# Kernel tuning notes

Measured on AMD Instinct MI355X. Metric: run time of the kernel, lower is better.

## Reference

```python
import jax, jax.numpy as jnp
import numpy as np
from jax import lax

# module hyperparameters (init_kwargs)
L2_U = 0.01
L2_V = 0.01
L1_RATIO = 0.1
EPS = 1e-16


def soft_thresholding(x, thr):
    return jnp.sign(x) * jnp.maximum(jnp.abs(x) - thr, 0.0)


def update_u(x, u, v, l1, l2):
    # x: [B, M, N], u: [B, M, R], v: [B, N, R]
    a = x @ v                              # [B, M, R]
    b = jnp.swapaxes(v, -1, -2) @ v        # [B, R, R]
    R = u.shape[-1]

    # Sequential coordinate descent over rank r; u_new carries the data
    # dependency. term2 over indices j != r equals u_new @ b[:, :, r]
    # minus the diagonal contribution u_new[:, :, r] * b[r, r].
    def step(u_new, r):
        a_r = lax.dynamic_slice_in_dim(a, r, 1, 2)        # [B, M, 1]
        b_col = lax.dynamic_slice_in_dim(b, r, 1, 2)      # [B, R, 1]
        b_rr = lax.dynamic_slice_in_dim(b_col, r, 1, 1)   # [B, 1, 1]
        u_r = lax.dynamic_slice_in_dim(u_new, r, 1, 2)    # [B, M, 1]
        term2 = u_new @ b_col - u_r * b_rr                # [B, M, 1]
        num = soft_thresholding(a_r - term2, l1)
        ur_new = num / (b_rr + l2 + EPS)                  # project = Identity
        u_new = lax.dynamic_update_slice_in_dim(u_new, ur_new, r, 2)
        return u_new, None

    u_new, _ = lax.scan(step, u, jnp.arange(R))
    return u_new


def setup_inputs() -> dict:
    key = jax.random.key(0)
    kx, ku, kv = jax.random.split(key, 3)
    B, M, N, R = 16, 2048, 2048, 64
    x = jax.random.normal(kx, (B, M, N), dtype=jnp.float32)
    u = jax.random.normal(ku, (B, M, R), dtype=jnp.float32)
    v = jax.random.normal(kv, (B, N, R), dtype=jnp.float32)
    return {"x": x, "u": u, "v": v}


def reference(x, u, v):
    M, N = x.shape[-2], x.shape[-1]
    l1_u = L2_U * L1_RATIO * N
    l2_u = L2_U * (1.0 - L1_RATIO) * N
    l1_v = L2_V * L1_RATIO * M
    l2_v = L2_V * (1.0 - L1_RATIO) * M
    u = update_u(x, u, v, l1_u, l2_u)                       # factor 0
    v = update_u(jnp.swapaxes(x, -1, -2), v, u, l1_v, l2_v)  # factor 1 (uses new u)
    return (u, v)
```

## Files before the change

kernel.cpp:

```cpp
#include <hip/hip_runtime.h>

typedef __attribute__((ext_vector_type(8))) short short8;
typedef __attribute__((ext_vector_type(4))) float f32x4;

#define BB 16
#define MM 2048
#define NN 2048

static __device__ __forceinline__ unsigned int cvtpk(float lo, float hi) {
  unsigned int r;
  asm("v_cvt_pk_bf16_f32 %0, %1, %2" : "=v"(r) : "v"(lo), "v"(hi));
  return r;
}

#define WAITV(N)                                            \
  do {                                                      \
    asm volatile("s_waitcnt vmcnt(" #N ")" ::: "memory");   \
    __builtin_amdgcn_sched_barrier(0);                      \
  } while (0)
#define BAR() __builtin_amdgcn_s_barrier()

__global__ void transpose_cvt(const float* __restrict__ in,
                              unsigned short* __restrict__ out, int nrows) {
  __shared__ float t[64][65];
  int b = blockIdx.y;
  int n0 = blockIdx.x * 64;
  int tid = threadIdx.x;
  int lane = tid & 63;
  int q = tid >> 6;
  const float* inb = in + ((size_t)b * nrows + n0) * 64;
#pragma unroll
  for (int i = 0; i < 16; ++i) {
    int n = q * 16 + i;
    t[n][lane] = inb[n * 64 + lane];
  }
  __syncthreads();
  unsigned short* outb = out + (size_t)b * 64 * nrows + n0;
  int pr = tid & 31, rq = tid >> 5;
#pragma unroll
  for (int i = 0; i < 8; ++i) {
    int r = rq + 8 * i;
    int n = 2 * pr;
    *(unsigned int*)(outb + (size_t)r * nrows + n) = cvtpk(t[n][r], t[n + 1][r]);
  }
}

#define CD_TAIL(U_OUT, L1, L2E)                                                 \
  __syncthreads();                                                              \
  float* lsa = (float*)smem;                              \
  float* lsb = (float*)(smem + 16384);                    \
  float* invv = (float*)(smem + 32768);                   \
  _Pragma("unroll")                                                             \
  for (int i = 0; i < 4; ++i) {                                                 \
    int ctv = (w + i) & 3;                                                      \
    _Pragma("unroll")                                                           \
    for (int j = 0; j < 4; ++j) {                                               \
      lsa[(w * 16 + 4 * g + j) * 64 + ctv * 16 + lr] = acc[i][j];               \
      lsb[(w * 16 + 4 * g + j) * 64 + ctv * 16 + lr] = gacc[i][j];              \
    }                                                                           \
  }                                                                             \
  __syncthreads();                                                              \
  if (tid < 64) invv[tid] = 1.0f / (lsb[tid * 65] + (L2E));                     \
  __syncthreads();                                                              \
  float aa[16];                                                                 \
  _Pragma("unroll")                                                             \
  for (int i = 0; i < 4; ++i)                                                   \
    *(f32x4*)(aa + 4 * i) = *(const f32x4*)(lsa + rrow * 64 + p * 16 + 4 * i);  \
  const float* bp = lsb + p * 16;                                               \
  _Pragma("unroll")                                                             \
  for (int rr = 0; rr < 64; ++rr) {                                             \
    f32x4 b0 = *(const f32x4*)(bp + rr * 64);                                   \
    f32x4 b1 = *(const f32x4*)(bp + rr * 64 + 4);                               \
    f32x4 b2 = *(const f32x4*)(bp + rr * 64 + 8);                               \
    f32x4 b3 = *(const f32x4*)(bp + rr * 64 + 12);                              \
    float s0 = 0.f, s1 = 0.f, s2 = 0.f, s3 = 0.f;                               \
    _Pragma("unroll")                                                           \
    for (int i = 0; i < 4; ++i) {                                               \
      s0 = fmaf(uu[i], b0[i], s0);                                              \
      s1 = fmaf(uu[4 + i], b1[i], s1);                                          \
      s2 = fmaf(uu[8 + i], b2[i], s2);                                          \
      s3 = fmaf(uu[12 + i], b3[i], s3);                                         \
    }                                                                           \
    float s = (s0 + s1) + (s2 + s3);                                            \
    s += __shfl_xor(s, 1);                                                      \
    s += __shfl_xor(s, 2);                                                      \
    float brr = lsb[rr * 65];                                                   \
    float num = fmaf(uu[rr & 15], brr, aa[rr & 15] - s);                        \
    float cl = fminf(fmaxf(num, -(L1)), (L1));                                  \
    float nv = (num - cl) * invv[rr];                                           \
    if (p == (rr >> 4)) uu[rr & 15] = nv;                                       \
  }                                                                             \
  _Pragma("unroll")                                                             \
  for (int i = 0; i < 4; ++i)                                                   \
    *(f32x4*)((U_OUT) + ubase + 4 * i) = *(const f32x4*)(uu + 4 * i);

__global__ void __launch_bounds__(256, 2)
xv_cd(const float* __restrict__ x, const unsigned short* __restrict__ vT,
      const float* __restrict__ u_in, float* __restrict__ u_out,
      unsigned short* __restrict__ uT, float l1, float l2e) {
  __shared__ char smem[73728];
  int flat = blockIdx.x + gridDim.x * blockIdx.y;
  int b = ((flat >> 8) << 3) | (flat & 7);
  int tile0 = ((flat >> 3) & 31) * 64;
  int tid = threadIdx.x;
  int w = tid >> 6, l = tid & 63;
  int lr = l & 15, g = l >> 4;
  int rrow = tid >> 2, p = tid & 3;
  size_t ubase = ((size_t)b * MM + tile0 + rrow) * 64 + p * 16;
  float uu[16];
#pragma unroll
  for (int i = 0; i < 4; ++i)
    *(f32x4*)(uu + 4 * i) = *(const f32x4*)(u_in + ubase + 4 * i);

  const unsigned short* vb = vT + (size_t)b * 64 * NN;
  const char* xg0 = (const char*)x + ((size_t)b * MM + tile0) * (size_t)(NN * 4);
  f32x4 acc[4] = {};
  f32x4 gacc[4] = {};
  int rowb = (w * 16 + lr) * 256;
  int key = lr & 7;

#define XVSTAGE(DB, CH)                                                         \
  {                                                                             \
    char* lbs = (char*)smem + (DB)*16384;                                       \
    _Pragma("unroll")                                                           \
    for (int i = 0; i < 4; ++i) {                                               \
      int s = w * 4 + i;                                                        \
      int lg = ((l & 15) ^ ((s & 1) * 4 + (l >> 4))) * 16;                      \
      const char* gp = xg0 + (size_t)(s * 4 + (l >> 4)) * (NN * 4) +            \
                       (CH)*256 + lg;                                           \
      __builtin_amdgcn_global_load_lds(                                         \
          (const __attribute__((address_space(1))) unsigned int*)gp,            \
          (__attribute__((address_space(3))) unsigned int*)(lbs + s * 1024),    \
          16, 0, 0);                                                            \
    }                                                                           \
    char* bbs = (char*)smem + 49152 + (DB)*8192;                                \
    _Pragma("unroll")                                                           \
    for (int i = 0; i < 2; ++i) {                                               \
      int bi = w * 2 + i;                                                       \
      int row = bi * 8 + (l >> 3);                                              \
      int q8 = l & 7;                                                           \
      const char* gp = (const char*)vb + (size_t)row * (NN * 2) + (CH)*128 +    \
                       ((q8 ^ (row & 7)) * 16);                                 \
      __builtin_amdgcn_global_load_lds(                                         \
          (const __attribute__((address_space(1))) unsigned int*)gp,            \
          (__attribute__((address_space(3))) unsigned int*)(bbs + bi * 1024),   \
          16, 0, 0);                                                            \
    }                                                                           \
  }

#define XVCOMP(DB, CH)                                                          \
  {                                                                             \
    const char* lb = (const char*)smem + (DB)*16384 + rowb;                     \
    const char* Bb = (const char*)smem + 49152 + (DB)*8192;                     \
    _Pragma("unroll")                                                           \
    for (int kh = 0; kh < 2; ++kh) {                                            \
      f32x4 lo = *(const f32x4*)(lb + ((kh * 8 + 2 * g + 0) ^ key) * 16);       \
      f32x4 hi = *(const f32x4*)(lb + ((kh * 8 + 2 * g + 1) ^ key) * 16);       \
      union { short8 s; unsigned int u[4]; } af;                                \
      af.u[0] = cvtpk(lo[0], lo[1]);                                            \
      af.u[1] = cvtpk(lo[2], lo[3]);                                            \
      af.u[2] = cvtpk(hi[0], hi[1]);                                            \
      af.u[3] = cvtpk(hi[2], hi[3]);                                            \
      short8 bfbuf[4];                                                          \
      _Pragma("unroll")                                                         \
      for (int i = 0; i < 4; ++i) {                                             \
        int row = ((w + i) & 3) * 16 + lr;                                      \
        bfbuf[i] = *(const short8*)(Bb + row * 128 +                            \
                                    (((kh * 4 + g) ^ (row & 7)) * 16));         \
      }                                                                         \
      _Pragma("unroll")                                                         \
      for (int i = 0; i < 4; ++i)                                               \
        acc[i] = __builtin_amdgcn_mfma_f32_16x16x32_bf16(af.s, bfbuf[i],        \
                                                         acc[i], 0, 0, 0);      \
      _Pragma("unroll")                                                         \
      for (int i = 0; i < 4; ++i)                                               \
        gacc[i] = __builtin_amdgcn_mfma_f32_16x16x32_bf16(bfbuf[0], bfbuf[i],   \
                                                          gacc[i], 0, 0, 0);    \
    }                                                                           \
  }

  XVSTAGE(0, 0);
  XVSTAGE(1, 1);
  {
    int cur = 0, stg = 2;
    for (int c = 0; c < 30; ++c) {
      WAITV(6); BAR();
      XVSTAGE(stg, c + 2);
      XVCOMP(cur, c);
      cur = (cur == 2) ? 0 : cur + 1;
      stg = (stg == 2) ? 0 : stg + 1;
    }
    WAITV(6); BAR(); XVCOMP(cur, 30);
    cur = (cur == 2) ? 0 : cur + 1;
    WAITV(0); BAR(); XVCOMP(cur, 31);
  }
#undef XVSTAGE
#undef XVCOMP

  CD_TAIL(u_out, l1, l2e)

  __syncthreads();
  float* t65 = (float*)smem;
#pragma unroll
  for (int i = 0; i < 16; ++i) t65[rrow * 65 + p * 16 + i] = uu[i];
  __syncthreads();
  unsigned short* outb = uT + (size_t)b * 64 * MM + tile0;
  int q = tid & 31, h2 = (tid >> 5) & 1, seg = tid >> 6;
#pragma unroll
  for (int cc = 0; cc < 8; ++cc) {
    int c0 = seg * 16 + cc * 2 + h2;
    *(unsigned int*)(outb + (size_t)c0 * MM + 2 * q) =
        cvtpk(t65[(2 * q) * 65 + c0], t65[(2 * q + 1) * 65 + c0]);
  }
}

__global__ void __launch_bounds__(256, 2)
xtu_cd(const float* __restrict__ x, const unsigned short* __restrict__ uT,
       const float* __restrict__ v_in, float* __restrict__ v_out,
       float l1, float l2e) {
  __shared__ char smem[73728];
  int flat = blockIdx.x + gridDim.x * blockIdx.y;
  int b = (BB - 1) - (((flat >> 8) << 3) | (flat & 7));
  int tile0 = ((flat >> 3) & 31) * 64;
  int tid = threadIdx.x;
  int w = tid >> 6, l = tid & 63;
  int lr = l & 15, g = l >> 4;
  int rrow = tid >> 2, p = tid & 3;
  size_t ubase = ((size_t)b * NN + tile0 + rrow) * 64 + p * 16;
  float uu[16];
#pragma unroll
  for (int i = 0; i < 4; ++i)
    *(f32x4*)(uu + 4 * i) = *(const f32x4*)(v_in + ubase + 4 * i);

  const unsigned short* ub = uT + (size_t)b * 64 * MM;
  const char* xg0 = (const char*)x + ((size_t)b * MM * NN + tile0) * 4;
  f32x4 acc[4] = {};
  f32x4 gacc[4] = {};
  int slotX = ((w * 4 + (lr >> 2)) ^ ((g & 1) << 2)) * 16 + (lr & 3) * 4;

#define XTSTAGE(DB, CH)                                                         \
  {                                                                             \
    char* lbs = (char*)smem + (DB)*16384;                                       \
    _Pragma("unroll")                                                           \
    for (int i = 0; i < 4; ++i) {                                               \
      int s = w * 4 + i;                                                        \
      int lg = ((l & 15) ^ (((s >> 1) & 1) << 2)) * 16;                         \
      const char* gp = xg0 + (size_t)((CH)*64 + s * 4 + (l >> 4)) * (NN * 4) +  \
                       lg;                                                      \
      __builtin_amdgcn_global_load_lds(                                         \
          (const __attribute__((address_space(1))) unsigned int*)gp,            \
          (__attribute__((address_space(3))) unsigned int*)(lbs + s * 1024),    \
          16, 0, 0);                                                            \
    }                                                                           \
    char* bbs = (char*)smem + 49152 + (DB)*8192;                                \
    _Pragma("unroll")                                                           \
    for (int i = 0; i < 2; ++i) {                                               \
      int bi = w * 2 + i;                                                       \
      int row = bi * 8 + (l >> 3);                                              \
      int q8 = l & 7;                                                           \
      const char* gp = (const char*)ub + (size_t)row * (MM * 2) + (CH)*128 +    \
                       ((q8 ^ (row & 7)) * 16);                                 \
      __builtin_amdgcn_global_load_lds(                                         \
          (const __attribute__((address_space(1))) unsigned int*)gp,            \
          (__attribute__((address_space(3))) unsigned int*)(bbs + bi * 1024),   \
          16, 0, 0);                                                            \
    }                                                                           \
  }

#define XTCOMP(DB, CH)                                                          \
  {                                                                             \
    const char* lb = (const char*)smem + (DB)*16384 + slotX;                    \
    const char* Bb = (const char*)smem + 49152 + (DB)*8192;                     \
    _Pragma("unroll")                                                           \
    for (int kh = 0; kh < 2; ++kh) {                                            \
      const char* lk = lb + (kh * 32 + 8 * g) * 256;                            \
      float vv[8];                                                              \
      _Pragma("unroll")                                                         \
      for (int j = 0; j < 8; ++j)                                               \
        vv[j] = *(const float*)(lk + j * 256);                                  \
      union { short8 s; unsigned int u[4]; } af;                                \
      af.u[0] = cvtpk(vv[0], vv[1]);                                            \
      af.u[1] = cvtpk(vv[2], vv[3]);                                            \
      af.u[2] = cvtpk(vv[4], vv[5]);                                            \
      af.u[3] = cvtpk(vv[6], vv[7]);                                            \
      short8 bfbuf[4];                                                          \
      _Pragma("unroll")                                                         \
      for (int i = 0; i < 4; ++i) {                                             \
        int row = ((w + i) & 3) * 16 + lr;                                      \
        bfbuf[i] = *(const short8*)(Bb + row * 128 +                            \
                                    (((kh * 4 + g) ^ (row & 7)) * 16));         \
      }                                                                         \
      _Pragma("unroll")                                                         \
      for (int i = 0; i < 4; ++i)                                               \
        acc[i] = __builtin_amdgcn_mfma_f32_16x16x32_bf16(af.s, bfbuf[i],        \
                                                         acc[i], 0, 0, 0);      \
      _Pragma("unroll")                                                         \
      for (int i = 0; i < 4; ++i)                                               \
        gacc[i] = __builtin_amdgcn_mfma_f32_16x16x32_bf16(bfbuf[0], bfbuf[i],   \
                                                          gacc[i], 0, 0, 0);    \
    }                                                                           \
  }

  XTSTAGE(0, 0);
  XTSTAGE(1, 1);
  {
    int cur = 0, stg = 2;
    for (int c = 0; c < 30; ++c) {
      WAITV(6); BAR();
      XTSTAGE(stg, c + 2);
      XTCOMP(cur, c);
      cur = (cur == 2) ? 0 : cur + 1;
      stg = (stg == 2) ? 0 : stg + 1;
    }
    WAITV(6); BAR(); XTCOMP(cur, 30);
    cur = (cur == 2) ? 0 : cur + 1;
    WAITV(0); BAR(); XTCOMP(cur, 31);
  }
#undef XTSTAGE
#undef XTCOMP

  CD_TAIL(v_out, l1, l2e)
}

extern "C" void kernel_launch(void* const* d_in, const int* in_sizes, int n_in,
                              void* d_out, int out_size, void* d_ws, size_t ws_size,
                              hipStream_t stream) {
  (void)in_sizes; (void)n_in; (void)out_size; (void)ws_size;
  const float* x = (const float*)d_in[0];
  const float* u = (const float*)d_in[1];
  const float* v = (const float*)d_in[2];
  float* u_out = (float*)d_out;
  float* v_out = u_out + (size_t)BB * MM * 64;

  unsigned short* tTv = (unsigned short*)d_ws;
  unsigned short* tTu = tTv + (size_t)BB * 64 * NN;

  float l1u = (float)(0.01 * 0.1 * (double)NN);
  float l2u = (float)(0.01 * 0.9 * (double)NN + 1e-16);
  float l1v = (float)(0.01 * 0.1 * (double)MM);
  float l2v = (float)(0.01 * 0.9 * (double)MM + 1e-16);

  transpose_cvt<<<dim3(NN / 64, BB), 256, 0, stream>>>(v, tTv, NN);
  xv_cd<<<dim3(MM / 64, BB), 256, 0, stream>>>(x, tTv, u, u_out, tTu, l1u, l2u);
  xtu_cd<<<dim3(NN / 64, BB), 256, 0, stream>>>(x, tTu, v, v_out, l1v, l2v);
}
```

Baseline: 124.6 us.

## Load x tiles straight into registers instead of staging through LDS

```diff
diff --git a/kernel.cpp b/kernel.cpp
--- a/kernel.cpp
+++ b/kernel.cpp
@@ -98,7 +98,7 @@
 xv_cd(const float* __restrict__ x, const unsigned short* __restrict__ vT,
       const float* __restrict__ u_in, float* __restrict__ u_out,
       unsigned short* __restrict__ uT, float l1, float l2e) {
-  __shared__ char smem[73728];
+  __shared__ char smem[36864];
   int flat = blockIdx.x + gridDim.x * blockIdx.y;
   int b = ((flat >> 8) << 3) | (flat & 7);
   int tile0 = ((flat >> 3) & 31) * 64;
@@ -114,26 +114,14 @@
 
   const unsigned short* vb = vT + (size_t)b * 64 * NN;
   const char* xg0 = (const char*)x + ((size_t)b * MM + tile0) * (size_t)(NN * 4);
+  const char* xrow = xg0 + (size_t)(w * 16 + lr) * (NN * 4) + g * 32;
   f32x4 acc[4] = {};
   f32x4 gacc[4] = {};
-  int rowb = (w * 16 + lr) * 256;
-  int key = lr & 7;
-
-#define XVSTAGE(DB, CH)                                                         \
-  {                                                                             \
-    char* lbs = (char*)smem + (DB)*16384;                                       \
-    _Pragma("unroll")                                                           \
-    for (int i = 0; i < 4; ++i) {                                               \
-      int s = w * 4 + i;                                                        \
-      int lg = ((l & 15) ^ ((s & 1) * 4 + (l >> 4))) * 16;                      \
-      const char* gp = xg0 + (size_t)(s * 4 + (l >> 4)) * (NN * 4) +            \
-                       (CH)*256 + lg;                                           \
-      __builtin_amdgcn_global_load_lds(                                         \
-          (const __attribute__((address_space(1))) unsigned int*)gp,            \
-          (__attribute__((address_space(3))) unsigned int*)(lbs + s * 1024),    \
-          16, 0, 0);                                                            \
-    }                                                                           \
-    char* bbs = (char*)smem + 49152 + (DB)*8192;                                \
+  f32x4 pA[4], pB[4], pC[4];
+
+#define BSTAGE(DB, CH)                                                          \
+  {                                                                             \
+    char* bbs = (char*)smem + (DB)*8192;                                        \
     _Pragma("unroll")                                                           \
     for (int i = 0; i < 2; ++i) {                                               \
       int bi = w * 2 + i;                                                       \
@@ -148,19 +136,25 @@
     }                                                                           \
   }
 
-#define XVCOMP(DB, CH)                                                          \
-  {                                                                             \
-    const char* lb = (const char*)smem + (DB)*16384 + rowb;                     \
-    const char* Bb = (const char*)smem + 49152 + (DB)*8192;                     \
+#define ALOAD(P, CH)                                                            \
+  {                                                                             \
+    const char* ga = xrow + (CH)*256;                                           \
+    P[0] = *(const f32x4*)(ga);                                                 \
+    P[1] = *(const f32x4*)(ga + 16);                                            \
+    P[2] = *(const f32x4*)(ga + 128);                                           \
+    P[3] = *(const f32x4*)(ga + 144);                                           \
+  }
+
+#define XVCOMP(DB, P, CH)                                                       \
+  {                                                                             \
+    const char* Bb = (const char*)smem + (DB)*8192;                             \
     _Pragma("unroll")                                                           \
     for (int kh = 0; kh < 2; ++kh) {                                            \
-      f32x4 lo = *(const f32x4*)(lb + ((kh * 8 + 2 * g + 0) ^ key) * 16);       \
-      f32x4 hi = *(const f32x4*)(lb + ((kh * 8 + 2 * g + 1) ^ key) * 16);       \
       union { short8 s; unsigned int u[4]; } af;                                \
-      af.u[0] = cvtpk(lo[0], lo[1]);                                            \
-      af.u[1] = cvtpk(lo[2], lo[3]);                                            \
-      af.u[2] = cvtpk(hi[0], hi[1]);                                            \
-      af.u[3] = cvtpk(hi[2], hi[3]);                                            \
+      af.u[0] = cvtpk(P[2 * kh + 0][0], P[2 * kh + 0][1]);                      \
+      af.u[1] = cvtpk(P[2 * kh + 0][2], P[2 * kh + 0][3]);                      \
+      af.u[2] = cvtpk(P[2 * kh + 1][0], P[2 * kh + 1][1]);                      \
+      af.u[3] = cvtpk(P[2 * kh + 1][2], P[2 * kh + 1][3]);                      \
       short8 bfbuf[4];                                                          \
       _Pragma("unroll")                                                         \
       for (int i = 0; i < 4; ++i) {                                             \
@@ -179,22 +173,17 @@
     }                                                                           \
   }
 
-  XVSTAGE(0, 0);
-  XVSTAGE(1, 1);
-  {
-    int cur = 0, stg = 2;
-    for (int c = 0; c < 30; ++c) {
-      WAITV(6); BAR();
-      XVSTAGE(stg, c + 2);
-      XVCOMP(cur, c);
-      cur = (cur == 2) ? 0 : cur + 1;
-      stg = (stg == 2) ? 0 : stg + 1;
-    }
-    WAITV(6); BAR(); XVCOMP(cur, 30);
-    cur = (cur == 2) ? 0 : cur + 1;
-    WAITV(0); BAR(); XVCOMP(cur, 31);
-  }
-#undef XVSTAGE
+  BSTAGE(0, 0); ALOAD(pA, 0);
+  BSTAGE(1, 1); ALOAD(pB, 1);
+  for (int cc = 0; cc < 30; cc += 3) {
+    WAITV(6); BAR(); BSTAGE(2, cc + 2); ALOAD(pC, cc + 2); XVCOMP(0, pA, cc);
+    WAITV(6); BAR(); BSTAGE(0, cc + 3); ALOAD(pA, cc + 3); XVCOMP(1, pB, cc + 1);
+    WAITV(6); BAR(); BSTAGE(1, cc + 4); ALOAD(pB, cc + 4); XVCOMP(2, pC, cc + 2);
+  }
+  WAITV(6); BAR(); XVCOMP(0, pA, 30);
+  WAITV(0); BAR(); XVCOMP(1, pB, 31);
+#undef BSTAGE
+#undef ALOAD
 #undef XVCOMP
 
   CD_TAIL(u_out, l1, l2e)
```

New measurement: 125.4 us. Within noise of the previous version (+0.6%).
